# Optimization experiments

Measured on AMD Instinct MI355X. Metric: run time of the kernel, lower is better.

Reference implementation:

```python
import jax, jax.numpy as jnp
import numpy as np

B, S, D = 4, 2048, 1024
H = 8
HD = D // H          # head_dim = 128
SCALE = 1.0 / np.sqrt(HD)


def setup_inputs() -> dict:
    key = jax.random.key(0)
    ks = jax.random.split(key, 9)
    def lin_w(k):
        return jax.random.normal(k, (D, D), dtype=jnp.float32) * (1.0 / np.sqrt(D))
    return {
        "hidden_states": jax.random.normal(ks[0], (B, S, D), dtype=jnp.float32),
        "Wq": lin_w(ks[1]), "bq": jax.random.normal(ks[2], (D,), dtype=jnp.float32) * 0.02,
        "Wk": lin_w(ks[3]), "bk": jax.random.normal(ks[4], (D,), dtype=jnp.float32) * 0.02,
        "Wv": lin_w(ks[5]), "bv": jax.random.normal(ks[6], (D,), dtype=jnp.float32) * 0.02,
        "Wo": lin_w(ks[7]), "bo": jax.random.normal(ks[8], (D,), dtype=jnp.float32) * 0.02,
    }


def reference(hidden_states, Wq, bq, Wk, bk, Wv, bv, Wo, bo):
    b, s, _ = hidden_states.shape
    # Linear projections (torch nn.Linear: x @ W.T + b; here W stored as (D, D) acting as W.T)
    Q = hidden_states @ Wq + bq
    K = hidden_states @ Wk + bk
    V = hidden_states @ Wv + bv
    # (b, h, s, hd)
    Q = Q.reshape(b, s, H, HD).transpose(0, 2, 1, 3)
    K = K.reshape(b, s, H, HD).transpose(0, 2, 1, 3)
    V = V.reshape(b, s, H, HD).transpose(0, 2, 1, 3)
    # Quaternion inner product sum_quat Re(k* \otimes q) == plain dot product over head_dim:
    # conjugation negates (x,y,z) and the Hamilton real part w1w2 - x1x2 - y1y2 - z1z2
    # re-negates them, yielding wK wQ + xK xQ + yK yQ + zK zQ per quaternion.
    scores = jnp.einsum("bhqd,bhkd->bhqk", Q, K) * SCALE
    attn = jax.nn.softmax(scores, axis=-1)
    out = jnp.einsum("bhqk,bhkd->bhqd", attn, V)
    out = out.transpose(0, 2, 1, 3).reshape(b, s, D)
    return out @ Wo + bo
```

## Files before the change

kernel.cpp:

```cpp
#include <hip/hip_runtime.h>

typedef _Float16 h8 __attribute__((ext_vector_type(8)));
typedef _Float16 h4 __attribute__((ext_vector_type(4)));
typedef float fx4 __attribute__((ext_vector_type(4)));

#define D_ 1024
#define S_ 2048
#define H_ 8
#define HD_ 128
static constexpr float SCALE = 0.0883883476483184405f;
static constexpr float LOG2E = 1.44269504088896f;
static constexpr float M0C = 5.0f * 1.44269504088896f;

typedef __attribute__((address_space(3))) void lds_void_t;
typedef __attribute__((address_space(1))) void g_void_t;

__device__ __forceinline__ void gl_lds16(const void* g, void* l) {
  __builtin_amdgcn_global_load_lds((const g_void_t*)(uintptr_t)g,
                                   (lds_void_t*)(uintptr_t)l, 16, 0, 0);
}

__device__ __forceinline__ float fast_exp2(float x) {
#if __has_builtin(__builtin_amdgcn_exp2f)
  return __builtin_amdgcn_exp2f(x);
#else
  return __expf(x * 0.6931471805599453f);
#endif
}

__global__ void prep_kernel(const float* __restrict__ hs, _Float16* __restrict__ hs_h,
                            const float* __restrict__ W0, const float* __restrict__ W1,
                            const float* __restrict__ W2, const float* __restrict__ W3,
                            _Float16* __restrict__ Wt) {
  int bid = blockIdx.x, tid = threadIdx.x;
  if (bid < 4096) {
    int i = bid * 256 + tid;
    float4 v0 = ((const float4*)hs)[2 * i];
    float4 v1 = ((const float4*)hs)[2 * i + 1];
    h8 o = { (_Float16)v0.x, (_Float16)v0.y, (_Float16)v0.z, (_Float16)v0.w,
             (_Float16)v1.x, (_Float16)v1.y, (_Float16)v1.z, (_Float16)v1.w };
    ((h8*)hs_h)[i] = o;
    return;
  }
  __shared__ float tile[32][33];
  int zz = bid - 4096;
  int wz = zz >> 10, rem = zz & 1023;
  const float* W = (wz == 0) ? W0 : (wz == 1) ? W1 : (wz == 2) ? W2 : W3;
  _Float16* dst = Wt + (size_t)wz * D_ * D_;
  int bx = (rem & 31) * 32, by = (rem >> 5) * 32;
  int tx = tid & 31, ty = tid >> 5;
  for (int i = ty; i < 32; i += 8)
    tile[i][tx] = W[(by + i) * D_ + bx + tx];
  __syncthreads();
  int ri = tid >> 3, cg = tid & 7;
  h4 o = { (_Float16)tile[cg * 4 + 0][ri], (_Float16)tile[cg * 4 + 1][ri],
           (_Float16)tile[cg * 4 + 2][ri], (_Float16)tile[cg * 4 + 3][ri] };
  *(h4*)&dst[(size_t)(bx + ri) * D_ + by + cg * 4] = o;
}

__global__ void transpose_v(const _Float16* __restrict__ Vh, _Float16* __restrict__ Vt) {
  __shared__ _Float16 tile[32][36];
  int s0 = blockIdx.x * 32, d0 = blockIdx.y * 32;
  int bh = blockIdx.z;
  int b = bh >> 3, h = bh & 7;
  int t = threadIdx.x;
  int si = t >> 3, dg = t & 7;
  *(ushort4*)&tile[si][dg * 4] =
      *(const ushort4*)&Vh[(size_t)(b * S_ + s0 + si) * D_ + h * HD_ + d0 + dg * 4];
  __syncthreads();
  int di = t >> 3, sg = t & 7;
  h4 o = { tile[sg * 4 + 0][di], tile[sg * 4 + 1][di],
           tile[sg * 4 + 2][di], tile[sg * 4 + 3][di] };
  *(h4*)&Vt[(size_t)(bh * HD_ + d0 + di) * S_ + s0 + sg * 4] = o;
}

template <typename OutT>
__device__ __forceinline__ void gemm_body(const _Float16* __restrict__ A,
                                          const _Float16* __restrict__ Bt,
                                          const float* __restrict__ bias,
                                          OutT* __restrict__ C, int m0, int n0) {
  constexpr int K = 1024, N = 1024;
  __shared__ __align__(16) _Float16 As[128 * 64];
  __shared__ __align__(16) _Float16 Bs[128 * 64];
  int tid = threadIdx.x;
  int lane = tid & 63, w = tid >> 6;
  int wr = w >> 1, wc = w & 1;
  int l16 = lane & 15, quad = lane >> 4;
  fx4 acc[4][4] = {};
  for (int k0 = 0; k0 < K; k0 += 64) {
#pragma unroll
    for (int it = 0; it < 4; ++it) {
      int s = it * 256 + tid;
      int row = s >> 3, gc = (s & 7) ^ (row & 7);
      gl_lds16(&A[(m0 + row) * K + k0 + gc * 8], &As[s * 8]);
      gl_lds16(&Bt[(n0 + row) * K + k0 + gc * 8], &Bs[s * 8]);
    }
    __syncthreads();
#pragma unroll
    for (int kk = 0; kk < 2; ++kk) {
      h8 a[4], b[4];
#pragma unroll
      for (int i = 0; i < 4; ++i) {
        int row = wr * 64 + i * 16 + l16;
        a[i] = *(const h8*)&As[(row * 8 + ((kk * 4 + quad) ^ (row & 7))) * 8];
      }
#pragma unroll
      for (int j = 0; j < 4; ++j) {
        int row = wc * 64 + j * 16 + l16;
        b[j] = *(const h8*)&Bs[(row * 8 + ((kk * 4 + quad) ^ (row & 7))) * 8];
      }
#pragma unroll
      for (int i = 0; i < 4; ++i)
#pragma unroll
        for (int j = 0; j < 4; ++j)
          acc[i][j] = __builtin_amdgcn_mfma_f32_16x16x32_f16(a[i], b[j], acc[i][j], 0, 0, 0);
    }
    __syncthreads();
  }
#pragma unroll
  for (int i = 0; i < 4; ++i) {
    int row = m0 + wr * 64 + i * 16 + quad * 4;
#pragma unroll
    for (int j = 0; j < 4; ++j) {
      int col = n0 + wc * 64 + j * 16 + l16;
      float bv_ = bias[col];
#pragma unroll
      for (int r = 0; r < 4; ++r)
        C[(row + r) * N + col] = (OutT)(acc[i][j][r] + bv_);
    }
  }
}

__global__ __launch_bounds__(256) void gemm_qkv(const _Float16* __restrict__ A,
                                                const _Float16* __restrict__ Wt,
                                                const float* __restrict__ bq,
                                                const float* __restrict__ bk,
                                                const float* __restrict__ bv,
                                                _Float16* __restrict__ QKV) {
  int lin = blockIdx.x;
  int xcd = lin & 7, idx = lin >> 3;
  int z = idx >> 6, r = idx & 63;
  int mt = xcd * 8 + (r >> 3);
  int nt = r & 7;
  const float* bias = (z == 0) ? bq : ((z == 1) ? bk : bv);
  gemm_body<_Float16>(A, Wt + z * (D_ * D_), bias, QKV + z * (S_ * 4 * D_),
                      mt * 128, nt * 128);
}

__global__ __launch_bounds__(256) void gemm_out(const _Float16* __restrict__ A,
                                                const _Float16* __restrict__ Wt,
                                                const float* __restrict__ bias,
                                                float* __restrict__ C) {
  int lin = blockIdx.x;
  int xcd = lin & 7, idx = lin >> 3;
  int mt = xcd * 8 + (idx >> 3);
  int nt = idx & 7;
  gemm_body<float>(A, Wt, bias, C, mt * 128, nt * 128);
}

__global__ __launch_bounds__(256, 2) void attn_kernel(const _Float16* __restrict__ Qh,
                                                      const _Float16* __restrict__ Kh,
                                                      const _Float16* __restrict__ Vt,
                                                      _Float16* __restrict__ Oh) {
  __shared__ __align__(16) _Float16 Ks[2][64 * 128];
  __shared__ __align__(16) _Float16 Vs[2][128 * 64];
  const int tid = threadIdx.x;
  const int lane = tid & 63, w = tid >> 6;
  const int l16 = lane & 15, quad = lane >> 4;
  const int glane = (l16 & 3) | (((l16 >> 2) & 1) << 2);

  const int lin = blockIdx.y * gridDim.x + blockIdx.x;
  const int xcd = lin & 7, idx = lin >> 3;
  const int bh = (idx >> 4) * 8 + xcd;
  const int qblk = idx & 15;
  const int b = bh >> 3, h = bh & 7;
  const int q0 = qblk * 128 + w * 32;

  const _Float16* Qp = Qh + (size_t)(b * S_ + q0) * D_ + h * HD_;
  const _Float16* Kp = Kh + (size_t)(b * S_) * D_ + h * HD_;
  const _Float16* Vp = Vt + (size_t)bh * HD_ * S_;

  int kOff[4], vOff[4], ldsOff[4];
#pragma unroll
  for (int it = 0; it < 4; ++it) {
    int s = it * 256 + tid;
    int rowK = s >> 4;
    int gK = (rowK & 3) | (((rowK >> 3) & 1) << 2);
    int gcK = (s & 15) ^ gK;
    kOff[it] = rowK * D_ + gcK * 8;
    int rowV = s >> 3, gcV = (s & 7) ^ (rowV & 7);
    vOff[it] = rowV * S_ + gcV * 8;
    ldsOff[it] = s * 8;
  }

  h8 aq[2][4];
#pragma unroll
  for (int nt = 0; nt < 2; ++nt)
#pragma unroll
    for (int kf = 0; kf < 4; ++kf) {
      h8 v = *(const h8*)&Qp[(nt * 16 + l16) * D_ + kf * 32 + quad * 8];
      aq[nt][kf] = v * (_Float16)(SCALE * LOG2E);
    }

  fx4 o[2][8] = {};
  float lp[2] = {0.f, 0.f};
  h8 pkA[2][2], pkB[2][2];

#define ATTN_STEP(T, CB, PROD, CONS, DOPV, DOPRE)                              \
  {                                                                            \
    __syncthreads();                                                           \
    if (DOPRE) {                                                               \
      _Pragma("unroll") for (int it = 0; it < 4; ++it)                         \
          gl_lds16(Kp + ((T) + 1) * 64 * D_ + kOff[it],                        \
                   &Ks[(CB) ^ 1][ldsOff[it]]);                                 \
    }                                                                          \
    _Pragma("unroll") for (int it = 0; it < 4; ++it)                           \
        gl_lds16(Vp + (T) * 64 + vOff[it], &Vs[CB][ldsOff[it]]);               \
    fx4 st[4][2];                                                              \
    _Pragma("unroll") for (int blk = 0; blk < 4; ++blk)                        \
        _Pragma("unroll") for (int nt = 0; nt < 2; ++nt)                       \
            st[blk][nt] = (fx4){-M0C, -M0C, -M0C, -M0C};                       \
    __builtin_amdgcn_s_setprio(1);                                             \
    _Pragma("unroll") for (int blk = 0; blk < 4; ++blk) {                      \
      int row_ = (blk >> 1) * 32 + (l16 >> 2) * 8 + (blk & 1) * 4 + (l16 & 3); \
      h8 ak[4];                                                                \
      _Pragma("unroll") for (int kf = 0; kf < 4; ++kf)                         \
          ak[kf] =                                                             \
              *(const h8*)&Ks[CB][(row_ * 16 + ((kf * 4 + quad) ^ glane)) * 8];\
      _Pragma("unroll") for (int kf = 0; kf < 4; ++kf) {                       \
        st[blk][0] = __builtin_amdgcn_mfma_f32_16x16x32_f16(ak[kf], aq[0][kf], \
                                                            st[blk][0], 0, 0, 0); \
        st[blk][1] = __builtin_amdgcn_mfma_f32_16x16x32_f16(ak[kf], aq[1][kf], \
                                                            st[blk][1], 0, 0, 0); \
      }                                                                        \
    }                                                                          \
    if (DOPV) {                                                                \
      _Pragma("unroll") for (int ntd = 0; ntd < 8; ++ntd) {                    \
        int rowd = ntd * 16 + l16;                                             \
        _Pragma("unroll") for (int kc = 0; kc < 2; ++kc) {                     \
          h8 bv = *(const h8*)&Vs[(CB) ^ 1]                                    \
              [(rowd * 8 + ((kc * 4 + quad) ^ (rowd & 7))) * 8];               \
          o[0][ntd] = __builtin_amdgcn_mfma_f32_16x16x32_f16(CONS[kc][0], bv,  \
                                                             o[0][ntd], 0, 0, 0); \
          o[1][ntd] = __builtin_amdgcn_mfma_f32_16x16x32_f16(CONS[kc][1], bv,  \
                                                             o[1][ntd], 0, 0, 0); \
        }                                                                      \
      }                                                                        \
    }                                                                          \
    __builtin_amdgcn_s_setprio(0);                                             \
    _Pragma("unroll") for (int blk = 0; blk < 4; ++blk) {                      \
      const int kc_ = blk >> 1, jh_ = (blk & 1) * 4;                           \
      _Pragma("unroll") for (int nt = 0; nt < 2; ++nt) {                       \
        float p0 = fast_exp2(st[blk][nt][0]);                                  \
        float p1 = fast_exp2(st[blk][nt][1]);                                  \
        float p2 = fast_exp2(st[blk][nt][2]);                                  \
        float p3 = fast_exp2(st[blk][nt][3]);                                  \
        lp[nt] += (p0 + p1) + (p2 + p3);                                       \
        PROD[kc_][nt][jh_ + 0] = (_Float16)p0;                                 \
        PROD[kc_][nt][jh_ + 1] = (_Float16)p1;                                 \
        PROD[kc_][nt][jh_ + 2] = (_Float16)p2;                                 \
        PROD[kc_][nt][jh_ + 3] = (_Float16)p3;                                 \
      }                                                                        \
    }                                                                          \
  }

#pragma unroll
  for (int it = 0; it < 4; ++it)
    gl_lds16(Kp + kOff[it], &Ks[0][ldsOff[it]]);

  ATTN_STEP(0, 0, pkA, pkB, false, true)
  for (int t2 = 1; t2 < 31; t2 += 2) {
    ATTN_STEP(t2, 1, pkB, pkA, true, true)
    ATTN_STEP(t2 + 1, 0, pkA, pkB, true, true)
  }
  ATTN_STEP(31, 1, pkB, pkA, true, false)
#undef ATTN_STEP

  __syncthreads();

#pragma unroll
  for (int ntd = 0; ntd < 8; ++ntd) {
    int rowd = ntd * 16 + l16;
#pragma unroll
    for (int kc = 0; kc < 2; ++kc) {
      h8 bv = *(const h8*)&Vs[1][(rowd * 8 + ((kc * 4 + quad) ^ (rowd & 7))) * 8];
      o[0][ntd] = __builtin_amdgcn_mfma_f32_16x16x32_f16(pkB[kc][0], bv, o[0][ntd], 0, 0, 0);
      o[1][ntd] = __builtin_amdgcn_mfma_f32_16x16x32_f16(pkB[kc][1], bv, o[1][ntd], 0, 0, 0);
    }
  }

#pragma unroll
  for (int nt = 0; nt < 2; ++nt) {
    float v = lp[nt];
    v += __shfl_xor(v, 16);
    v += __shfl_xor(v, 32);
    lp[nt] = v;
  }
#pragma unroll
  for (int mi = 0; mi < 2; ++mi)
#pragma unroll
    for (int r = 0; r < 4; ++r) {
      float lsum = __shfl(lp[mi], quad * 4 + r);
      float inv = 1.0f / lsum;
      int row = q0 + mi * 16 + quad * 4 + r;
      _Float16* op = Oh + (size_t)(b * S_ + row) * D_ + h * HD_;
#pragma unroll
      for (int nt = 0; nt < 8; ++nt)
        op[nt * 16 + l16] = (_Float16)(o[mi][nt][r] * inv);
    }
}

extern "C" void kernel_launch(void* const* d_in, const int* in_sizes, int n_in,
                              void* d_out, int out_size, void* d_ws, size_t ws_size,
                              hipStream_t stream) {
  const float* hs = (const float*)d_in[0];
  const float* Wq = (const float*)d_in[1];
  const float* bq = (const float*)d_in[2];
  const float* Wk = (const float*)d_in[3];
  const float* bk = (const float*)d_in[4];
  const float* Wv = (const float*)d_in[5];
  const float* bv = (const float*)d_in[6];
  const float* Wo = (const float*)d_in[7];
  const float* bo = (const float*)d_in[8];
  float* out = (float*)d_out;

  const int MD = S_ * 4 * D_;
  const int WD = D_ * D_;
  _Float16* ws = (_Float16*)d_ws;
  _Float16* hs_h = ws;
  _Float16* WtQ = hs_h + MD;
  _Float16* WtO = WtQ + 3 * WD;
  _Float16* QKVh = WtO + WD;
  _Float16* Vt = QKVh + 3 * MD;
  _Float16* Oh = Vt + MD;

  prep_kernel<<<8192, 256, 0, stream>>>(hs, hs_h, Wq, Wk, Wv, Wo, WtQ);
  gemm_qkv<<<1536, 256, 0, stream>>>(hs_h, WtQ, bq, bk, bv, QKVh);
  transpose_v<<<dim3(S_ / 32, HD_ / 32, 32), 256, 0, stream>>>(QKVh + 2 * MD, Vt);
  attn_kernel<<<dim3(S_ / 128, 32), 256, 0, stream>>>(QKVh, QKVh + MD, Vt, Oh);
  gemm_out<<<512, 256, 0, stream>>>(Oh, WtO, bo, out);
}
```

Before: 268.6 us.

## Load V tiles directly from global into registers instead of staging through LDS

Removes the double-buffered V shared-memory tile and its async global-to-LDS copies. Each wave now loads its V fragments straight from global memory into a register array one step ahead of the PV MFMAs. This frees half the LDS and cuts LDS read traffic, but each of the four waves in a block redundantly fetches the full V tile from global/L2 and the extra 64 registers may hurt occupancy or cause spills. The global load latency is only partly hidden behind the softmax exp work.

```diff
diff --git a/kernel.cpp b/kernel.cpp
--- a/kernel.cpp
+++ b/kernel.cpp
@@ -163,7 +163,6 @@
                                                       const _Float16* __restrict__ Vt,
                                                       _Float16* __restrict__ Oh) {
   __shared__ __align__(16) _Float16 Ks[2][64 * 128];
-  __shared__ __align__(16) _Float16 Vs[2][128 * 64];
   const int tid = threadIdx.x;
   const int lane = tid & 63, w = tid >> 6;
   const int l16 = lane & 15, quad = lane >> 4;
@@ -179,8 +178,9 @@
   const _Float16* Qp = Qh + (size_t)(b * S_ + q0) * D_ + h * HD_;
   const _Float16* Kp = Kh + (size_t)(b * S_) * D_ + h * HD_;
   const _Float16* Vp = Vt + (size_t)bh * HD_ * S_;
-
-  int kOff[4], vOff[4], ldsOff[4];
+  const _Float16* Vb = Vp + (size_t)l16 * S_ + quad * 8;
+
+  int kOff[4], ldsOff[4];
 #pragma unroll
   for (int it = 0; it < 4; ++it) {
     int s = it * 256 + tid;
@@ -188,8 +188,6 @@
     int gK = (rowK & 3) | (((rowK >> 3) & 1) << 2);
     int gcK = (s & 15) ^ gK;
     kOff[it] = rowK * D_ + gcK * 8;
-    int rowV = s >> 3, gcV = (s & 7) ^ (rowV & 7);
-    vOff[it] = rowV * S_ + gcV * 8;
     ldsOff[it] = s * 8;
   }
 
@@ -205,6 +203,7 @@
   fx4 o[2][8] = {};
   float lp[2] = {0.f, 0.f};
   h8 pkA[2][2], pkB[2][2];
+  h8 vr[8][2];
 
 #define ATTN_STEP(T, CB, PROD, CONS, DOPV, DOPRE)                              \
   {                                                                            \
@@ -214,8 +213,6 @@
           gl_lds16(Kp + ((T) + 1) * 64 * D_ + kOff[it],                        \
                    &Ks[(CB) ^ 1][ldsOff[it]]);                                 \
     }                                                                          \
-    _Pragma("unroll") for (int it = 0; it < 4; ++it)                           \
-        gl_lds16(Vp + (T) * 64 + vOff[it], &Vs[CB][ldsOff[it]]);               \
     fx4 st[4][2];                                                              \
     _Pragma("unroll") for (int blk = 0; blk < 4; ++blk)                        \
         _Pragma("unroll") for (int nt = 0; nt < 2; ++nt)                       \
@@ -236,18 +233,20 @@
     }                                                                          \
     if (DOPV) {                                                                \
       _Pragma("unroll") for (int ntd = 0; ntd < 8; ++ntd) {                    \
-        int rowd = ntd * 16 + l16;                                             \
         _Pragma("unroll") for (int kc = 0; kc < 2; ++kc) {                     \
-          h8 bv = *(const h8*)&Vs[(CB) ^ 1]                                    \
-              [(rowd * 8 + ((kc * 4 + quad) ^ (rowd & 7))) * 8];               \
-          o[0][ntd] = __builtin_amdgcn_mfma_f32_16x16x32_f16(CONS[kc][0], bv,  \
-                                                             o[0][ntd], 0, 0, 0); \
-          o[1][ntd] = __builtin_amdgcn_mfma_f32_16x16x32_f16(CONS[kc][1], bv,  \
-                                                             o[1][ntd], 0, 0, 0); \
+          o[0][ntd] = __builtin_amdgcn_mfma_f32_16x16x32_f16(CONS[kc][0],      \
+                                            vr[ntd][kc], o[0][ntd], 0, 0, 0); \
+          o[1][ntd] = __builtin_amdgcn_mfma_f32_16x16x32_f16(CONS[kc][1],      \
+                                            vr[ntd][kc], o[1][ntd], 0, 0, 0); \
         }                                                                      \
       }                                                                        \
     }                                                                          \
     __builtin_amdgcn_s_setprio(0);                                             \
+                      \
+    _Pragma("unroll") for (int ntd = 0; ntd < 8; ++ntd)                        \
+        _Pragma("unroll") for (int kc = 0; kc < 2; ++kc)                       \
+            vr[ntd][kc] = *(const h8*)&Vb[(size_t)ntd * 16 * S_ +              \
+                                          (T) * 64 + kc * 32];                 \
     _Pragma("unroll") for (int blk = 0; blk < 4; ++blk) {                      \
       const int kc_ = blk >> 1, jh_ = (blk & 1) * 4;                           \
       _Pragma("unroll") for (int nt = 0; nt < 2; ++nt) {                       \
@@ -280,12 +279,10 @@
 
 #pragma unroll
   for (int ntd = 0; ntd < 8; ++ntd) {
-    int rowd = ntd * 16 + l16;
 #pragma unroll
     for (int kc = 0; kc < 2; ++kc) {
-      h8 bv = *(const h8*)&Vs[1][(rowd * 8 + ((kc * 4 + quad) ^ (rowd & 7))) * 8];
-      o[0][ntd] = __builtin_amdgcn_mfma_f32_16x16x32_f16(pkB[kc][0], bv, o[0][ntd], 0, 0, 0);
-      o[1][ntd] = __builtin_amdgcn_mfma_f32_16x16x32_f16(pkB[kc][1], bv, o[1][ntd], 0, 0, 0);
+      o[0][ntd] = __builtin_amdgcn_mfma_f32_16x16x32_f16(pkB[kc][0], vr[ntd][kc], o[0][ntd], 0, 0, 0);
+      o[1][ntd] = __builtin_amdgcn_mfma_f32_16x16x32_f16(pkB[kc][1], vr[ntd][kc], o[1][ntd], 0, 0, 0);
     }
   }
 
```

After: 386.4 us. 1.44x slower.
